# Kernel optimization log

Hardware: AMD Instinct MI355X
Metric: run time of the kernel (lower is better)

## Reference

```python
import jax, jax.numpy as jnp
import numpy as np

D_MODEL = 1024
NUM_HEADS = 16
D_FF = 4096
SEQ = 2048
BATCH = 2
THETA = 10000.0
EPS = 1e-5


def _param(key, shape, fan_in, fan_out):
    std = 2.0 / (fan_in + fan_out) ** 0.5
    return std * jax.random.truncated_normal(key, -3.0, 3.0, shape, dtype=jnp.float32)


def setup_inputs() -> dict:
    key = jax.random.key(0)
    ks = jax.random.split(key, 8)
    d, h, f = D_MODEL, NUM_HEADS, D_FF
    return {
        'x': jax.random.normal(ks[0], (BATCH, SEQ, d), dtype=jnp.float32),
        'token_positions': jnp.arange(SEQ, dtype=jnp.int32),
        'wq': _param(ks[1], (d, d), d, d),
        'wk': _param(ks[2], (d, d), d, d),
        'wv': _param(ks[3], (d, d), d, d),
        'wo': _param(ks[4], (d, d), d, d),
        'ln1_w': jnp.ones((d,), jnp.float32),
        'ln2_w': jnp.ones((d,), jnp.float32),
        'w1': _param(ks[5], (f, d), d, f),
        'w2': _param(ks[6], (d, f), f, d),
        'w3': _param(ks[7], (f, d), d, f),
    }


def rmsnorm(x, w):
    x32 = x.astype(jnp.float32)
    rms = jnp.sqrt(jnp.mean(x32 * x32, axis=-1, keepdims=True) + EPS)
    return ((x32 / rms) * w).astype(x.dtype)


def apply_rope(x, cos, sin):
    # x: [b, h, s, d_k]; cos/sin: [s, d_k//2] -> broadcast as [1,1,s,d_k//2]
    xe, xo = x[..., ::2], x[..., 1::2]
    c = cos[None, None, :, :]
    s = sin[None, None, :, :]
    re = xe * c - xo * s
    ro = xe * s + xo * c
    return jnp.stack((re, ro), axis=-1).reshape(x.shape)


def block_forward(x, token_positions, wq, wk, wv, wo, ln1_w, ln2_w, w1, w2, w3):
    b, s, d = x.shape
    h = NUM_HEADS
    dk = d // h
    # RoPE tables at token positions
    inv_freq = 1.0 / (THETA ** (jnp.arange(0, dk // 2, dtype=jnp.float32) * 2.0 / dk))
    freqs = token_positions.astype(jnp.float32)[:, None] * inv_freq[None, :]  # [s, dk/2]
    cos, sin = jnp.cos(freqs), jnp.sin(freqs)

    # --- attention sublayer (pre-norm) ---
    xn = rmsnorm(x, ln1_w)
    q = jnp.einsum('bsd,ed->bse', xn, wq).reshape(b, s, h, dk).transpose(0, 2, 1, 3)
    k = jnp.einsum('bsd,ed->bse', xn, wk).reshape(b, s, h, dk).transpose(0, 2, 1, 3)
    v = jnp.einsum('bsd,ed->bse', xn, wv).reshape(b, s, h, dk).transpose(0, 2, 1, 3)
    q = apply_rope(q, cos, sin)
    k = apply_rope(k, cos, sin)
    scores = jnp.einsum('bhqd,bhkd->bhqk', q, k) / jnp.sqrt(jnp.float32(dk))
    causal = jnp.tril(jnp.ones((s, s), dtype=bool))
    scores = jnp.where(causal[None, None], scores, -jnp.inf)
    attn = jax.nn.softmax(scores, axis=-1)
    o = jnp.einsum('bhqk,bhkd->bhqd', attn, v)
    o = o.transpose(0, 2, 1, 3).reshape(b, s, d)
    x = x + jnp.einsum('bse,de->bsd', o, wo)

    # --- SwiGLU sublayer (pre-norm) ---
    xn = rmsnorm(x, ln2_w)
    x1 = jnp.einsum('bsd,fd->bsf', xn, w1)
    x3 = jnp.einsum('bsd,fd->bsf', xn, w3)
    gated = (x1 * jax.nn.sigmoid(x1)) * x3
    return x + jnp.einsum('bsf,df->bsd', gated, w2)


def reference(x, token_positions, wq, wk, wv, wo, ln1_w, ln2_w, w1, w2, w3):
    return block_forward(x, token_positions, wq, wk, wv, wo, ln1_w, ln2_w, w1, w2, w3)
```

## Files before the change

### kernel.cpp

```cpp
#include <hip/hip_runtime.h>
#include <hip/hip_bf16.h>

typedef __attribute__((ext_vector_type(4))) float f32x4;
typedef __attribute__((ext_vector_type(8))) short bf16x8;
typedef unsigned short u16;
typedef unsigned int u32;
typedef __attribute__((ext_vector_type(4))) u16 u16x4;

#define DEV static __device__ __forceinline__

constexpr int Bb = 2, Ss = 2048, Dd = 1024, Hh = 16, DKk = 64;
constexpr int Mm = Bb * Ss;

DEV float bf2f(u16 u) { union { u32 i; float f; } v; v.i = (u32)u << 16; return v.f; }
DEV u16 f2bf(float f) {
  union { float f; u32 i; } v; v.f = f;
  u32 r = v.i + 0x7FFFu + ((v.i >> 16) & 1u);
  return (u16)(r >> 16);
}

DEV void gload_lds16(const u16* g, u16* l) {
  __builtin_amdgcn_global_load_lds((const __attribute__((address_space(1))) u32*)g,
                                   (__attribute__((address_space(3))) u32*)l, 16, 0, 0);
}

__global__ void k_cvt_all(const float* __restrict__ wq, const float* __restrict__ wk,
                          const float* __restrict__ wv, const float* __restrict__ wo,
                          const float* __restrict__ w1, const float* __restrict__ w2,
                          const float* __restrict__ w3,
                          u16* __restrict__ wqkv, u16* __restrict__ wob,
                          u16* __restrict__ w13, u16* __restrict__ w2b) {
  int i = (blockIdx.x * 256 + threadIdx.x) * 4;
  int seg = i >> 20;
  const float* src; u16* dst;
  if (seg == 0)      { src = wq + i;             dst = wqkv + i; }
  else if (seg == 1) { src = wk + (i - (1<<20)); dst = wqkv + i; }
  else if (seg == 2) { src = wv + (i - (2<<20)); dst = wqkv + i; }
  else if (seg == 3) { src = wo + (i - (3<<20)); dst = wob  + (i - (3<<20)); }
  else if (seg < 8)  { src = w1 + (i - (4<<20)); dst = w13  + (i - (4<<20)); }
  else if (seg < 12) { src = w2 + (i - (8<<20)); dst = w2b  + (i - (8<<20)); }
  else               { src = w3 + (i - (12<<20)); dst = w13 + (4<<20) + (i - (12<<20)); }
  float4 v = *(const float4*)src;
  u16x4 o = { f2bf(v.x), f2bf(v.y), f2bf(v.z), f2bf(v.w) };
  *(u16x4*)dst = o;
}

__global__ __launch_bounds__(256) void k_rmsnorm(const float* __restrict__ x,
                                                 const float* __restrict__ w,
                                                 u16* __restrict__ out) {
  int row = blockIdx.x;
  int t = threadIdx.x;
  float4 v = ((const float4*)(x + (long)row * Dd))[t];
  float ss = v.x * v.x + v.y * v.y + v.z * v.z + v.w * v.w;
#pragma unroll
  for (int m = 32; m; m >>= 1) ss += __shfl_xor(ss, m, 64);
  __shared__ float red[4];
  if ((t & 63) == 0) red[t >> 6] = ss;
  __syncthreads();
  float tot = red[0] + red[1] + red[2] + red[3];
  float r = rsqrtf(tot * (1.0f / Dd) + 1e-5f);
  float4 wv = ((const float4*)w)[t];
  u16x4 o = { f2bf(v.x * r * wv.x), f2bf(v.y * r * wv.y),
              f2bf(v.z * r * wv.z), f2bf(v.w * r * wv.w) };
  ((u16x4*)(out + (long)row * Dd))[t] = o;
}

__global__ void k_rope(u16* __restrict__ q, u16* __restrict__ k, const int* __restrict__ tp) {
  int idx = blockIdx.x * 256 + threadIdx.x;
  if (idx >= Bb * Ss * Hh * 32) return;
  int p = idx & 31;
  int h = (idx >> 5) & 15;
  int row = idx >> 9;
  int s = row & (Ss - 1);
  float pos = (float)tp[s];
  float invf = __expf(-(float)p * (2.0f / DKk) * 9.2103403719761836f);
  float fr = pos * invf;
  float sn, cs;
  sincosf(fr, &sn, &cs);
  long base = (long)row * Dd + h * DKk + 2 * p;
  float xe = bf2f(q[base]), xo = bf2f(q[base + 1]);
  q[base]     = f2bf((xe * cs - xo * sn) * 0.125f);
  q[base + 1] = f2bf((xe * sn + xo * cs) * 0.125f);
  xe = bf2f(k[base]); xo = bf2f(k[base + 1]);
  k[base]     = f2bf(xe * cs - xo * sn);
  k[base + 1] = f2bf(xe * sn + xo * cs);
}

__global__ void k_gate(u16* __restrict__ x1, const u16* __restrict__ x3, int n) {
  int i = (blockIdx.x * 256 + threadIdx.x) * 4;
  if (i >= n) return;
  u16x4 a = *(u16x4*)(x1 + i);
  u16x4 b = *(const u16x4*)(x3 + i);
#pragma unroll
  for (int j = 0; j < 4; j++) {
    float v = bf2f(a[j]);
    float g = v / (1.0f + __expf(-v)) * bf2f(b[j]);
    a[j] = f2bf(g);
  }
  *(u16x4*)(x1 + i) = a;
}

template <int OM, bool RES>
__global__ __launch_bounds__(256) void k_gemm(const u16* __restrict__ A,
                                              const u16* __restrict__ Bm,
                                              void* __restrict__ Cout,
                                              const float* __restrict__ Rres,
                                              int N, int K) {
  __shared__ u16 Abuf[128 * 32];
  __shared__ u16 Bbuf[128 * 32];
  const int tid = threadIdx.x;
  const int wid = tid >> 6, lane = tid & 63;
  const int wm = wid >> 1, wn = wid & 1;
  const int lq = lane >> 4, ll = lane & 15;
  const int m0 = blockIdx.y * 128, n0 = blockIdx.x * 128;

  f32x4 acc[4][4] = {};

  const int srow = tid >> 2;
  const int scol = (tid & 3) * 8;
  const long aoff = (long)(m0 + srow) * K + scol;
  const long boff = (long)(n0 + srow) * K + scol;
  u16* aldsw = Abuf + wid * 512;
  u16* bldsw = Bbuf + wid * 512;

  for (int k0 = 0; k0 < K; k0 += 32) {
    __syncthreads();
    gload_lds16(A + aoff + k0, aldsw);
    gload_lds16(A + aoff + (long)64 * K + k0, aldsw + 2048);
    gload_lds16(Bm + boff + k0, bldsw);
    gload_lds16(Bm + boff + (long)64 * K + k0, bldsw + 2048);
    __syncthreads();
    bf16x8 af[4], bfr[4];
#pragma unroll
    for (int i = 0; i < 4; i++)
      af[i] = *(const bf16x8*)&Abuf[(wm * 64 + i * 16 + ll) * 32 + lq * 8];
#pragma unroll
    for (int j = 0; j < 4; j++)
      bfr[j] = *(const bf16x8*)&Bbuf[(wn * 64 + j * 16 + ll) * 32 + lq * 8];
#pragma unroll
    for (int i = 0; i < 4; i++)
#pragma unroll
      for (int j = 0; j < 4; j++)
        acc[i][j] = __builtin_amdgcn_mfma_f32_16x16x32_bf16(af[i], bfr[j], acc[i][j], 0, 0, 0);
  }

#pragma unroll
  for (int i = 0; i < 4; i++) {
    const int rowb = m0 + wm * 64 + i * 16 + lq * 4;
#pragma unroll
    for (int j = 0; j < 4; j++) {
      const int col = n0 + wn * 64 + j * 16 + ll;
#pragma unroll
      for (int r = 0; r < 4; r++) {
        int rr = rowb + r;
        float v = acc[i][j][r];
        if (RES) v += Rres[(long)rr * N + col];
        if (OM == 1) {
          ((float*)Cout)[(long)rr * N + col] = v;
        } else if (OM == 0) {
          ((u16*)Cout)[(long)rr * N + col] = f2bf(v);
        } else if (OM == 3) {
          if (col < 2048) {
            ((u16*)Cout)[(long)(col >> 10) * (Mm * 1024) + (long)rr * 1024 + (col & 1023)] = f2bf(v);
          } else {
            int d = col & 63, hh = (col >> 6) & 15;
            int b2 = rr >> 11, s2 = rr & (Ss - 1);
            ((u16*)Cout)[(long)(2 * Mm * 1024) + ((long)((b2 * Hh + hh) * DKk + d)) * Ss + s2] = f2bf(v);
          }
        } else {
          ((u16*)Cout)[(long)(col >> 12) * ((long)Mm * 4096) + (long)rr * 4096 + (col & 4095)] = f2bf(v);
        }
      }
    }
  }
}

constexpr int PPAD = 80;

DEV void attn_tile(const u16* __restrict__ Kc, const u16* __restrict__ Vc,
                   u16* __restrict__ myP, const bf16x8* qf, f32x4* accO,
                   float* mrow, float* lrow, int qloc, bool diag, int lq, int ll) {
  f32x4 sacc[4] = {};
#pragma unroll
  for (int fn = 0; fn < 4; fn++)
#pragma unroll
    for (int ks = 0; ks < 2; ks++) {
      bf16x8 kf = *(const bf16x8*)&Kc[(fn * 16 + ll) * 64 + (((ks * 4 + lq) ^ (ll & 7)) * 8)];
      sacc[fn] = __builtin_amdgcn_mfma_f32_16x16x32_bf16(qf[ks], kf, sacc[fn], 0, 0, 0);
    }
  float sv[4][4], pmax[4];
#pragma unroll
  for (int r = 0; r < 4; r++) pmax[r] = -1e30f;
#pragma unroll
  for (int fn = 0; fn < 4; fn++) {
    int kc = fn * 16 + ll;
#pragma unroll
    for (int r = 0; r < 4; r++) {
      float v = sacc[fn][r];
      if (diag && kc > qloc + r) v = -1e30f;
      sv[fn][r] = v;
      pmax[r] = fmaxf(pmax[r], v);
    }
  }
#pragma unroll
  for (int r = 0; r < 4; r++) {
#pragma unroll
    for (int m = 1; m < 16; m <<= 1) pmax[r] = fmaxf(pmax[r], __shfl_xor(pmax[r], m, 64));
  }
  float alpha[4], rsum[4];
#pragma unroll
  for (int r = 0; r < 4; r++) {
    float mnew = fmaxf(mrow[r], pmax[r]);
    alpha[r] = __expf(mrow[r] - mnew);
    mrow[r] = mnew;
    rsum[r] = 0.f;
  }
#pragma unroll
  for (int fn = 0; fn < 4; fn++) {
#pragma unroll
    for (int r = 0; r < 4; r++) {
      float p = __expf(sv[fn][r] - mrow[r]);
      rsum[r] += p;
      myP[(lq * 4 + r) * PPAD + fn * 16 + ll] = f2bf(p);
    }
  }
#pragma unroll
  for (int r = 0; r < 4; r++) {
#pragma unroll
    for (int m = 1; m < 16; m <<= 1) rsum[r] += __shfl_xor(rsum[r], m, 64);
    lrow[r] = lrow[r] * alpha[r] + rsum[r];
  }
#pragma unroll
  for (int fn = 0; fn < 4; fn++)
#pragma unroll
    for (int r = 0; r < 4; r++) accO[fn][r] *= alpha[r];
  bf16x8 pa[2];
#pragma unroll
  for (int ks = 0; ks < 2; ks++)
    pa[ks] = *(const bf16x8*)&myP[ll * PPAD + ks * 32 + lq * 8];
#pragma unroll
  for (int fn = 0; fn < 4; fn++)
#pragma unroll
    for (int ks = 0; ks < 2; ks++) {
      bf16x8 vf = *(const bf16x8*)&Vc[(fn * 16 + ll) * 64 + (((ks * 4 + lq) ^ (ll & 7)) * 8)];
      accO[fn] = __builtin_amdgcn_mfma_f32_16x16x32_bf16(pa[ks], vf, accO[fn], 0, 0, 0);
    }
}

__global__ __launch_bounds__(256) void k_attn(const u16* __restrict__ Q,
                                              const u16* __restrict__ Kb,
                                              const u16* __restrict__ VT,
                                              u16* __restrict__ O) {
  __shared__ u16 Kt[2][64 * 64];
  __shared__ u16 Vt[2][64 * 64];
  __shared__ u16 P[4][16 * PPAD];
  const int pair = blockIdx.x;
  const int bh = blockIdx.y;
  const int b = bh >> 4, h = bh & 15;
  const int tid = threadIdx.x;
  const int wid = tid >> 6, lane = tid & 63;
  const int lq = lane >> 4, ll = lane & 15;
  const int qtA = pair, qtB = 31 - pair;
  const int qr0A = qtA * 64 + wid * 16;
  const int qr0B = qtB * 64 + wid * 16;
  const int qloc = wid * 16 + lq * 4;
  const long qkbase = ((long)b * Ss) * Dd + h * DKk;
  const long vbase  = ((long)(b * Hh + h) * DKk) * Ss;
  const int nk = 32 - pair;

  const int slot0 = wid * 64 + lane;
  const int r0 = slot0 >> 3, c0 = (slot0 & 7) ^ (r0 & 7);
  const int slot1 = 256 + slot0;
  const int r1 = slot1 >> 3, c1 = (slot1 & 7) ^ (r1 & 7);
  const int ldsb0 = (wid * 64) * 8;
  const int ldsb1 = (256 + wid * 64) * 8;

  bf16x8 qfA[2], qfB[2];
#pragma unroll
  for (int ks = 0; ks < 2; ks++) {
    qfA[ks] = *(const bf16x8*)&Q[qkbase + (long)(qr0A + ll) * Dd + ks * 32 + lq * 8];
    qfB[ks] = *(const bf16x8*)&Q[qkbase + (long)(qr0B + ll) * Dd + ks * 32 + lq * 8];
  }

  f32x4 accA[4] = {}, accB[4] = {};
  float mA[4], lA[4], mB[4], lB[4];
#pragma unroll
  for (int r = 0; r < 4; r++) { mA[r] = mB[r] = -1e30f; lA[r] = lB[r] = 0.f; }
  u16* myP = P[wid];

  gload_lds16(Kb + qkbase + (long)r0 * Dd + c0 * 8, Kt[0] + ldsb0);
  gload_lds16(Kb + qkbase + (long)r1 * Dd + c1 * 8, Kt[0] + ldsb1);
  gload_lds16(VT + vbase + (long)r0 * Ss + c0 * 8, Vt[0] + ldsb0);
  gload_lds16(VT + vbase + (long)r1 * Ss + c1 * 8, Vt[0] + ldsb1);
  __syncthreads();

  for (int kt = 0; kt < nk; kt++) {
    if (kt + 1 < nk) {
      const int kn = (kt + 1) * 64;
      u16* kd = Kt[(kt + 1) & 1];
      u16* vd = Vt[(kt + 1) & 1];
      gload_lds16(Kb + qkbase + (long)(kn + r0) * Dd + c0 * 8, kd + ldsb0);
      gload_lds16(Kb + qkbase + (long)(kn + r1) * Dd + c1 * 8, kd + ldsb1);
      gload_lds16(VT + vbase + (long)r0 * Ss + kn + c0 * 8, vd + ldsb0);
      gload_lds16(VT + vbase + (long)r1 * Ss + kn + c1 * 8, vd + ldsb1);
    }
    const u16* Kc = Kt[kt & 1];
    const u16* Vc = Vt[kt & 1];

    attn_tile(Kc, Vc, myP, qfB, accB, mB, lB, qloc, kt == nk - 1, lq, ll);
    if (kt <= pair)
      attn_tile(Kc, Vc, myP, qfA, accA, mA, lA, qloc, kt == pair, lq, ll);
    __syncthreads();
  }

#pragma unroll
  for (int fn = 0; fn < 4; fn++) {
#pragma unroll
    for (int r = 0; r < 4; r++) {
      int rowA = qr0A + lq * 4 + r;
      int rowB = qr0B + lq * 4 + r;
      O[((long)(b * Ss + rowA)) * Dd + h * DKk + fn * 16 + ll] = f2bf(accA[fn][r] / lA[r]);
      O[((long)(b * Ss + rowB)) * Dd + h * DKk + fn * 16 + ll] = f2bf(accB[fn][r] / lB[r]);
    }
  }
}

extern "C" void kernel_launch(void* const* d_in, const int* in_sizes, int n_in,
                              void* d_out, int out_size, void* d_ws, size_t ws_size,
                              hipStream_t stream) {
  const float* x   = (const float*)d_in[0];
  const int*   tp  = (const int*)d_in[1];
  const float* wq  = (const float*)d_in[2];
  const float* wk  = (const float*)d_in[3];
  const float* wv  = (const float*)d_in[4];
  const float* wo  = (const float*)d_in[5];
  const float* ln1 = (const float*)d_in[6];
  const float* ln2 = (const float*)d_in[7];
  const float* w1  = (const float*)d_in[8];
  const float* w2  = (const float*)d_in[9];
  const float* w3  = (const float*)d_in[10];

  char* ws = (char*)d_ws;
  const size_t MB = 1024 * 1024;
  u16*   wqkv_b = (u16*)(ws + 0 * MB);
  u16*   wo_b   = (u16*)(ws + 6 * MB);
  u16*   w13_b  = (u16*)(ws + 8 * MB);
  u16*   w2_b   = (u16*)(ws + 24 * MB);
  u16*   xn     = (u16*)(ws + 32 * MB);
  float* x2     = (float*)(ws + 40 * MB);
  u16*   qb     = (u16*)(ws + 56 * MB);
  u16*   kb     = (u16*)(ws + 64 * MB);
  u16*   vtb    = (u16*)(ws + 72 * MB);
  u16*   ob     = (u16*)(ws + 80 * MB);
  u16*   x1     = (u16*)(ws + 56 * MB);
  u16*   x3     = (u16*)(ws + 88 * MB);

  k_cvt_all<<<16384, 256, 0, stream>>>(wq, wk, wv, wo, w1, w2, w3,
                                       wqkv_b, wo_b, w13_b, w2_b);
  k_rmsnorm<<<Mm, 256, 0, stream>>>(x, ln1, xn);
  k_gemm<3, false><<<dim3(24, 32), 256, 0, stream>>>(xn, wqkv_b, qb, nullptr, 3072, 1024);
  k_rope<<<(Bb * Ss * Hh * 32) / 256, 256, 0, stream>>>(qb, kb, tp);
  k_attn<<<dim3(16, 32), 256, 0, stream>>>(qb, kb, vtb, ob);
  k_gemm<1, true><<<dim3(8, 32), 256, 0, stream>>>(ob, wo_b, x2, x, 1024, 1024);
  k_rmsnorm<<<Mm, 256, 0, stream>>>(x2, ln2, xn);
  k_gemm<4, false><<<dim3(64, 32), 256, 0, stream>>>(xn, w13_b, x1, nullptr, 8192, 1024);
  k_gate<<<16384, 256, 0, stream>>>(x1, x3, 4096 * 4096);
  k_gemm<1, true><<<dim3(8, 32), 256, 0, stream>>>(x1, w2_b, (float*)d_out, x2, 1024, 4096);
}
```

Before: 386.3 us.

## Add 256x256 eight-wave pipelined GEMM for QKV and W1/W3 projections

Introduces a new 512-thread GEMM kernel with 256x256 output tiles, XOR-swizzled LDS staging through direct global-to-LDS loads, double buffering, and an interleaved phase schedule that overlaps next-tile loads with MFMA work. It uses explicit vmcnt waits, barriers and setprio around the MFMA blocks. The kernel replaces the older 128x128 GEMM for the QKV and fused W1/W3 projections, aiming for more data reuse per tile and better hiding of load latency. Costs are a large accumulator register footprint, lower occupancy, and fragile hand-tuned wait counts.

```diff
diff --git a/kernel.cpp b/kernel.cpp
--- a/kernel.cpp
+++ b/kernel.cpp
@@ -22,6 +22,10 @@
 DEV void gload_lds16(const u16* g, u16* l) {
   __builtin_amdgcn_global_load_lds((const __attribute__((address_space(1))) u32*)g,
                                    (__attribute__((address_space(3))) u32*)l, 16, 0, 0);
+}
+
+DEV int swz16(int o) {
+  return o ^ (((o >> 8) & 1) << 6) ^ (((o >> 9) & 1) << 5);
 }
 
 __global__ void k_cvt_all(const float* __restrict__ wq, const float* __restrict__ wk,
@@ -157,22 +161,134 @@
         if (RES) v += Rres[(long)rr * N + col];
         if (OM == 1) {
           ((float*)Cout)[(long)rr * N + col] = v;
-        } else if (OM == 0) {
+        } else {
           ((u16*)Cout)[(long)rr * N + col] = f2bf(v);
-        } else if (OM == 3) {
-          if (col < 2048) {
-            ((u16*)Cout)[(long)(col >> 10) * (Mm * 1024) + (long)rr * 1024 + (col & 1023)] = f2bf(v);
-          } else {
-            int d = col & 63, hh = (col >> 6) & 15;
-            int b2 = rr >> 11, s2 = rr & (Ss - 1);
-            ((u16*)Cout)[(long)(2 * Mm * 1024) + ((long)((b2 * Hh + hh) * DKk + d)) * Ss + s2] = f2bf(v);
-          }
-        } else {
-          ((u16*)Cout)[(long)(col >> 12) * ((long)Mm * 4096) + (long)rr * 4096 + (col & 4095)] = f2bf(v);
         }
       }
     }
   }
+}
+
+#define STG_A(d, h, kt)                                                         \
+  { gload_lds16(A + aoff[0] + (long)(h) * 128 * K + (kt) * 64, &sA[d][h][dst0]); \
+    gload_lds16(A + aoff[1] + (long)(h) * 128 * K + (kt) * 64, &sA[d][h][dst1]); }
+#define STG_B(d, h, kt)                                                         \
+  { gload_lds16(Bm + boff[0] + (long)(h) * 128 * K + (kt) * 64, &sB[d][h][dst0]); \
+    gload_lds16(Bm + boff[1] + (long)(h) * 128 * K + (kt) * 64, &sB[d][h][dst1]); }
+
+#define PHASE(q, d, DOB, WVN, ...)                                              \
+  {                                                                             \
+    bf16x8 af_[2][2];                                                           \
+    _Pragma("unroll") for (int s_ = 0; s_ < 2; s_++)                            \
+    _Pragma("unroll") for (int kk_ = 0; kk_ < 2; kk_++) {                       \
+      int ms_ = (q) * 4 + wm * 2 + s_;                                          \
+      int lo_ = ((ms_ & 7) * 16 + ll) * 128 + kk_ * 64 + lq * 16;               \
+      af_[s_][kk_] = *(const bf16x8*)((const char*)sA[d][ms_ >> 3] + swz16(lo_)); \
+    }                                                                           \
+    if (DOB) {                                                                  \
+      _Pragma("unroll") for (int ns_ = 0; ns_ < 4; ns_++)                       \
+      _Pragma("unroll") for (int kk_ = 0; kk_ < 2; kk_++) {                     \
+        int rl_ = wn * 64 + ns_ * 16 + ll;                                      \
+        int lo_ = (rl_ & 127) * 128 + kk_ * 64 + lq * 16;                       \
+        bfr[ns_][kk_] = *(const bf16x8*)((const char*)sB[d][rl_ >> 7] + swz16(lo_)); \
+      }                                                                         \
+    }                                                                           \
+    __VA_ARGS__;                                                                \
+    __builtin_amdgcn_s_barrier();                                               \
+    asm volatile("s_waitcnt lgkmcnt(0)" ::: "memory");                          \
+    __builtin_amdgcn_sched_barrier(0);                                          \
+    __builtin_amdgcn_s_setprio(1);                                              \
+    _Pragma("unroll") for (int s_ = 0; s_ < 2; s_++)                            \
+    _Pragma("unroll") for (int ns_ = 0; ns_ < 4; ns_++)                         \
+    _Pragma("unroll") for (int kk_ = 0; kk_ < 2; kk_++)                         \
+      acc[q][s_][ns_] = __builtin_amdgcn_mfma_f32_16x16x32_bf16(                \
+          af_[s_][kk_], bfr[ns_][kk_], acc[q][s_][ns_], 0, 0, 0);               \
+    __builtin_amdgcn_s_setprio(0);                                              \
+    { int wv_ = (WVN);                                                          \
+      if (wv_ == 6) { asm volatile("s_waitcnt vmcnt(6)" ::: "memory"); }        \
+      else if (wv_ == 0) { asm volatile("s_waitcnt vmcnt(0)" ::: "memory"); } } \
+    __builtin_amdgcn_s_barrier();                                               \
+  }
+
+template <int OM>
+__global__ __launch_bounds__(512) void k_gemm8(const u16* __restrict__ A,
+                                               const u16* __restrict__ Bm,
+                                               void* __restrict__ Cout,
+                                               int N, int K) {
+  __shared__ u16 sA[2][2][8192];
+  __shared__ u16 sB[2][2][8192];
+  const int nwg = gridDim.x * gridDim.y;
+  const int lin = blockIdx.y * gridDim.x + blockIdx.x;
+  const int swb = (lin & 7) * (nwg >> 3) + (lin >> 3);
+  const int bx = swb % gridDim.x, by = swb / gridDim.x;
+  const long m0 = (long)by * 256, n0 = (long)bx * 256;
+  const int tid = threadIdx.x;
+  const int wid = tid >> 6, lane = tid & 63;
+  const int wm = wid >> 2, wn = wid & 3;
+  const int lq = lane >> 4, ll = lane & 15;
+
+  long aoff[2], boff[2];
+#pragma unroll
+  for (int j = 0; j < 2; j++) {
+    int off = j * 8192 + wid * 1024 + lane * 16;
+    int lo = swz16(off);
+    int r = lo >> 7, c = (lo & 127) >> 1;
+    aoff[j] = (m0 + r) * K + c;
+    boff[j] = (n0 + r) * K + c;
+  }
+  const int dst0 = wid * 512;
+  const int dst1 = 4096 + wid * 512;
+
+  f32x4 acc[4][2][4] = {};
+  bf16x8 bfr[4][2];
+
+  const int NT = K >> 6;
+  const int NI = NT >> 1;
+
+  STG_A(0, 0, 0); STG_A(0, 1, 0); STG_B(0, 0, 0); STG_B(0, 1, 0);
+  STG_B(1, 0, 1); STG_B(1, 1, 1); STG_A(1, 0, 1);
+  asm volatile("s_waitcnt vmcnt(6)" ::: "memory");
+  __builtin_amdgcn_s_barrier();
+
+  for (int it = 0; it < NI; it++) {
+    const int t = 2 * it;
+    const bool full = (t + 2 < NT);
+    PHASE(0, 0, true,  -1,            STG_A(1, 1, t + 1))
+    PHASE(1, 0, false, -1,            if (full) STG_B(0, 0, t + 2))
+    PHASE(2, 0, false, -1,            if (full) STG_B(0, 1, t + 2))
+    PHASE(3, 0, false, full ? 6 : 0,  if (full) STG_A(0, 0, t + 2))
+    PHASE(0, 1, true,  -1,            if (full) STG_A(0, 1, t + 2))
+    PHASE(1, 1, false, -1,            if (full) STG_B(1, 0, t + 3))
+    PHASE(2, 1, false, -1,            if (full) STG_B(1, 1, t + 3))
+    PHASE(3, 1, false, full ? 6 : -1, if (full) STG_A(1, 0, t + 3))
+  }
+
+#pragma unroll
+  for (int q = 0; q < 4; q++)
+#pragma unroll
+    for (int s = 0; s < 2; s++) {
+      const long row0 = m0 + (q * 4 + wm * 2 + s) * 16 + lq * 4;
+#pragma unroll
+      for (int ns = 0; ns < 4; ns++) {
+        const long col = n0 + wn * 64 + ns * 16 + ll;
+#pragma unroll
+        for (int r = 0; r < 4; r++) {
+          float v = acc[q][s][ns][r];
+          long rr = row0 + r;
+          if (OM == 3) {
+            if (col < 2048) {
+              ((u16*)Cout)[(col >> 10) * (long)(Mm * 1024) + rr * 1024 + (col & 1023)] = f2bf(v);
+            } else {
+              int d = col & 63, hh = ((int)col >> 6) & 15;
+              int b2 = (int)rr >> 11, s2 = (int)rr & (Ss - 1);
+              ((u16*)Cout)[(long)(2 * Mm * 1024) + ((long)((b2 * Hh + hh) * DKk + d)) * Ss + s2] = f2bf(v);
+            }
+          } else {
+            ((u16*)Cout)[(col >> 12) * ((long)Mm * 4096) + rr * 4096 + (col & 4095)] = f2bf(v);
+          }
+        }
+      }
+    }
 }
 
 constexpr int PPAD = 80;
@@ -358,12 +474,12 @@
   k_cvt_all<<<16384, 256, 0, stream>>>(wq, wk, wv, wo, w1, w2, w3,
                                        wqkv_b, wo_b, w13_b, w2_b);
   k_rmsnorm<<<Mm, 256, 0, stream>>>(x, ln1, xn);
-  k_gemm<3, false><<<dim3(24, 32), 256, 0, stream>>>(xn, wqkv_b, qb, nullptr, 3072, 1024);
+  k_gemm8<3><<<dim3(12, 16), 512, 0, stream>>>(xn, wqkv_b, qb, 3072, 1024);
   k_rope<<<(Bb * Ss * Hh * 32) / 256, 256, 0, stream>>>(qb, kb, tp);
   k_attn<<<dim3(16, 32), 256, 0, stream>>>(qb, kb, vtb, ob);
   k_gemm<1, true><<<dim3(8, 32), 256, 0, stream>>>(ob, wo_b, x2, x, 1024, 1024);
   k_rmsnorm<<<Mm, 256, 0, stream>>>(x2, ln2, xn);
-  k_gemm<4, false><<<dim3(64, 32), 256, 0, stream>>>(xn, w13_b, x1, nullptr, 8192, 1024);
+  k_gemm8<4><<<dim3(32, 16), 512, 0, stream>>>(xn, w13_b, x1, 8192, 1024);
   k_gate<<<16384, 256, 0, stream>>>(x1, x3, 4096 * 4096);
   k_gemm<1, true><<<dim3(8, 32), 256, 0, stream>>>(x1, w2_b, (float*)d_out, x2, 1024, 4096);
 }
```

Measured after the change: 377.8 us. 1.02x faster.
